# Optimization experiments

Measured on AMD Instinct MI355X. Metric: run time of the kernel, lower is better.

The kernel has to match this reference:

```python
import jax, jax.numpy as jnp
import numpy as np

N_SRC, N_DST, E = 100000, 50000, 1000000
IN_F, H, D = 256, 4, 32
NEG_SLOPE = 0.2


def setup_inputs() -> dict:
    key = jax.random.key(0)
    k = jax.random.split(key, 7)
    x = jax.random.normal(k[0], (N_SRC, IN_F), dtype=jnp.float32)
    # scale weights so exp() of attention logits stays well-conditioned
    fc_w = jax.random.normal(k[1], (H * D, IN_F), dtype=jnp.float32) * (1.0 / np.sqrt(IN_F))
    attn_l = jax.random.normal(k[2], (1, H, D), dtype=jnp.float32) * 0.1
    attn_r = jax.random.normal(k[3], (1, H, D), dtype=jnp.float32) * 0.1
    src_idx = jax.random.randint(k[4], (E,), 0, N_SRC, dtype=jnp.int32)
    dst_idx = jax.random.randint(k[5], (E,), 0, N_DST, dtype=jnp.int32)
    dst_node_ids = jax.random.randint(k[6], (N_DST,), 0, N_SRC, dtype=jnp.int32)
    return {"x": x, "fc_w": fc_w, "attn_l": attn_l, "attn_r": attn_r,
            "src_idx": src_idx, "dst_idx": dst_idx, "dst_node_ids": dst_node_ids}


def reference(x, fc_w, attn_l, attn_r, src_idx, dst_idx, dst_node_ids):
    # fc: [N_src, in] @ [in, H*D] -> [N_src, H, D]
    h = (x @ fc_w.T).reshape(-1, H, D)
    # per-node, per-head attention scalars
    el = jnp.einsum('nhd,ohd->nh', h, attn_l)            # [N_src, H]
    h_dst = h[dst_node_ids]                               # self_gather -> [N_dst, H, D]
    er = jnp.einsum('nhd,ohd->nh', h_dst, attn_r)        # [N_dst, H]
    # apply_edge: e = el[src] + er[dst], then leaky_relu + exp (edge softmax numerator)
    e = el[src_idx] + er[dst_idx]                         # [E, H]
    e = jnp.where(e >= 0, e, NEG_SLOPE * e)
    exp_e = jnp.exp(e)
    # apply_node: segment-sum denominators over destination nodes
    sum_exp = jax.ops.segment_sum(exp_e, dst_idx, num_segments=N_DST)  # [N_dst, H]
    att = exp_e / sum_exp[dst_idx]                        # [E, H]
    # attention_gather: weighted scatter-add of source features to dst nodes
    msg = att[:, :, None] * h[src_idx]                    # [E, H, D]
    out = jax.ops.segment_sum(msg, dst_idx, num_segments=N_DST)        # [N_dst, H, D]
    return out.reshape(N_DST, H * D)
```

## Files before the change

### kernel.cpp

```cpp
#include <hip/hip_runtime.h>
#include <hip/hip_bf16.h>

#define N_SRC_N  100000
#define N_DST_N  50000
#define NE       1000000
#define IN_F     256
#define NH       4
#define ND       32
#define HD       128
#define NEG_SLOPE 0.2f

#define DPB      32
#define NB       1563
#define CAP      1024

typedef __attribute__((ext_vector_type(8))) short short8v;
typedef __attribute__((ext_vector_type(4))) short short4v;
typedef __attribute__((ext_vector_type(4))) float f32x4;

__device__ __forceinline__ short f2bf(float f) {
    __hip_bfloat16 h = __float2bfloat16(f);
    return *reinterpret_cast<short*>(&h);
}
__device__ __forceinline__ float bflo(unsigned u) { return __uint_as_float(u << 16); }
__device__ __forceinline__ float bfhi(unsigned u) { return __uint_as_float(u & 0xffff0000u); }

__device__ __forceinline__ void gl_lds16(const float* g, float* l) {
    __builtin_amdgcn_global_load_lds((const __attribute__((address_space(1))) unsigned*)g,
                                     (__attribute__((address_space(3))) unsigned*)l,
                                     16, 0, 0);
}

__global__ __launch_bounds__(256) void cvt_w(const float* __restrict__ w,
                                             short* __restrict__ wb)
{
    int i4 = blockIdx.x * 256 + threadIdx.x;
    if (i4 < (HD * IN_F) / 4) {
        f32x4 v = ((const f32x4*)w)[i4];
        short4v s;
        s[0] = f2bf(v[0]); s[1] = f2bf(v[1]); s[2] = f2bf(v[2]); s[3] = f2bf(v[3]);
        ((short4v*)wb)[i4] = s;
    }
}

__global__ __launch_bounds__(256) void gemm_fc_mfma(
    const float* __restrict__ x, const short* __restrict__ wb,
    const float* __restrict__ al, short* __restrict__ hb,
    float* __restrict__ el, int nrows)
{
    __shared__ float lds[2][64 * 64];

    const int w  = threadIdx.x >> 6;
    const int l  = threadIdx.x & 63;
    const int lr = l & 15;
    const int lk = l >> 4;
    const int row0 = blockIdx.x * 64;

    short8v bfr[2][8];
#pragma unroll
    for (int ct = 0; ct < 2; ++ct)
#pragma unroll
        for (int k = 0; k < 8; ++k)
            bfr[ct][k] = *(const short8v*)(wb + (size_t)(w * 32 + ct * 16 + lr) * IN_F
                                              + lk * 8 + k * 32);

    f32x4 acc[4][2];
#pragma unroll
    for (int rt = 0; rt < 4; ++rt)
#pragma unroll
        for (int ct = 0; ct < 2; ++ct) acc[rt][ct] = (f32x4){0.f, 0.f, 0.f, 0.f};

    auto stage = [&](int buf, int k0) {
#pragma unroll
        for (int i = 0; i < 4; ++i) {
            int chunk = i * 4 + w;
            int row   = chunk * 4 + (l >> 4);
            int srow  = row0 + row; if (srow > nrows - 1) srow = nrows - 1;
            int c_pos = (l & 15) * 16;
            int c_src = c_pos ^ ((row & 7) << 5);
            const float* g = x + (size_t)srow * IN_F + k0 + (c_src >> 2);
            gl_lds16(g, &lds[buf][chunk * 256]);
        }
    };

    stage(0, 0);
#pragma unroll
    for (int t = 0; t < 4; ++t) {
        __syncthreads();
        if (t < 3) stage((t + 1) & 1, (t + 1) * 64);
        const float* Lb = lds[t & 1];
#pragma unroll
        for (int kc = 0; kc < 2; ++kc) {
#pragma unroll
            for (int rt = 0; rt < 4; ++rt) {
                int row = rt * 16 + lr;
                int cb  = (kc * 128 + lk * 32) ^ ((row & 7) << 5);
                const float* p = Lb + row * 64 + (cb >> 2);
                f32x4 u0 = *(const f32x4*)p;
                f32x4 u1 = *(const f32x4*)(p + 4);
                short8v af;
                af[0] = f2bf(u0[0]); af[1] = f2bf(u0[1]);
                af[2] = f2bf(u0[2]); af[3] = f2bf(u0[3]);
                af[4] = f2bf(u1[0]); af[5] = f2bf(u1[1]);
                af[6] = f2bf(u1[2]); af[7] = f2bf(u1[3]);
                acc[rt][0] = __builtin_amdgcn_mfma_f32_16x16x32_bf16(
                                 af, bfr[0][t * 2 + kc], acc[rt][0], 0, 0, 0);
                acc[rt][1] = __builtin_amdgcn_mfma_f32_16x16x32_bf16(
                                 af, bfr[1][t * 2 + kc], acc[rt][1], 0, 0, 0);
            }
        }
    }

#pragma unroll
    for (int rt = 0; rt < 4; ++rt)
#pragma unroll
        for (int r = 0; r < 4; ++r) {
            int row = row0 + rt * 16 + lk * 4 + r;
            if (row < nrows) {
                short* hp = hb + (size_t)row * HD + w * 32 + lr;
                hp[0]  = f2bf(acc[rt][0][r]);
                hp[16] = f2bf(acc[rt][1][r]);
            }
        }

    float al0 = al[w * 32 + lr], al1 = al[w * 32 + 16 + lr];
#pragma unroll
    for (int rt = 0; rt < 4; ++rt) {
        float p[4];
#pragma unroll
        for (int r = 0; r < 4; ++r)
            p[r] = acc[rt][0][r] * al0 + acc[rt][1][r] * al1;
#pragma unroll
        for (int o = 1; o < 16; o <<= 1) {
#pragma unroll
            for (int r = 0; r < 4; ++r) p[r] += __shfl_xor(p[r], o, 64);
        }
        if (lr == 0) {
#pragma unroll
            for (int r = 0; r < 4; ++r) {
                int row = row0 + rt * 16 + lk * 4 + r;
                if (row < nrows) el[row * NH + w] = p[r];
            }
        }
    }
}

__global__ __launch_bounds__(256) void er_kernel(
    const short* __restrict__ hb, const float* __restrict__ ar,
    const int* __restrict__ dnid, float* __restrict__ er, int ndst)
{
    int i = blockIdx.x * 4 + (threadIdx.x >> 6);
    if (i >= ndst) return;
    int l = threadIdx.x & 63;
    int n = dnid[i];
    unsigned u = *(const unsigned*)(hb + (size_t)n * HD + 2 * l);
    float s = bflo(u) * ar[2 * l] + bfhi(u) * ar[2 * l + 1];
#pragma unroll
    for (int o = 1; o < 16; o <<= 1) s += __shfl_xor(s, o, 64);
    if ((l & 15) == 0) er[i * NH + (l >> 4)] = s;
}

__global__ __launch_bounds__(256) void bucket_hist(
    const int4* __restrict__ dst4, int* __restrict__ bcnt, int n4)
{
    __shared__ int lh[NB];
    for (int i = threadIdx.x; i < NB; i += 256) lh[i] = 0;
    __syncthreads();
#pragma unroll
    for (int q = 0; q < 4; ++q) {
        int e4 = blockIdx.x * 1024 + q * 256 + threadIdx.x;
        if (e4 < n4) {
            int4 v = dst4[e4];
            atomicAdd(&lh[v.x >> 5], 1); atomicAdd(&lh[v.y >> 5], 1);
            atomicAdd(&lh[v.z >> 5], 1); atomicAdd(&lh[v.w >> 5], 1);
        }
    }
    __syncthreads();
    for (int i = threadIdx.x; i < NB; i += 256) {
        int c = lh[i];
        if (c > 0) atomicAdd(&bcnt[i], c);
    }
}

__global__ __launch_bounds__(1024) void bucket_scan(
    const int* __restrict__ bcnt, int* __restrict__ boff, int* __restrict__ bcur, int n)
{
    int tid = threadIdx.x;
    int i0 = 2 * tid, i1 = 2 * tid + 1;
    int a = (i0 < n) ? bcnt[i0] : 0;
    int c = (i1 < n) ? bcnt[i1] : 0;
    int s = a + c, v = s;
#pragma unroll
    for (int o = 1; o < 64; o <<= 1) {
        int t = __shfl_up(v, o, 64);
        if ((tid & 63) >= o) v += t;
    }
    __shared__ int ws[16];
    if ((tid & 63) == 63) ws[tid >> 6] = v;
    __syncthreads();
    int add = 0;
    for (int q = 0; q < (tid >> 6); ++q) add += ws[q];
    int excl = v - s + add;
    if (i0 < n) { boff[i0] = excl;     bcur[i0] = excl; }
    if (i1 < n) { boff[i1] = excl + a; bcur[i1] = excl + a; }
}

__global__ __launch_bounds__(256) void partition(
    const int4* __restrict__ src4, const int4* __restrict__ dst4,
    int* __restrict__ bcur, int* __restrict__ ebuf, int n4)
{
    __shared__ int lh[NB];
    __shared__ int base[NB];
    for (int i = threadIdx.x; i < NB; i += 256) lh[i] = 0;
    __syncthreads();
    int4 sv[4], dv[4];
#pragma unroll
    for (int q = 0; q < 4; ++q) {
        int e4 = blockIdx.x * 1024 + q * 256 + threadIdx.x;
        if (e4 < n4) {
            sv[q] = src4[e4]; dv[q] = dst4[e4];
            atomicAdd(&lh[dv[q].x >> 5], 1); atomicAdd(&lh[dv[q].y >> 5], 1);
            atomicAdd(&lh[dv[q].z >> 5], 1); atomicAdd(&lh[dv[q].w >> 5], 1);
        } else {
            dv[q].x = -1;
        }
    }
    __syncthreads();
    for (int i = threadIdx.x; i < NB; i += 256) {
        int cnt = lh[i];
        base[i] = (cnt > 0) ? atomicAdd(&bcur[i], cnt) : 0;
        lh[i] = 0;
    }
    __syncthreads();
#pragma unroll
    for (int q = 0; q < 4; ++q) {
        if (dv[q].x < 0) continue;
        int ss[4] = {sv[q].x, sv[q].y, sv[q].z, sv[q].w};
        int dd[4] = {dv[q].x, dv[q].y, dv[q].z, dv[q].w};
#pragma unroll
        for (int j = 0; j < 4; ++j) {
            int b = dd[j] >> 5;
            int off = atomicAdd(&lh[b], 1);
            ebuf[base[b] + off] = ss[j] | ((dd[j] & 31) << 17);
        }
    }
}

__global__ __launch_bounds__(256) void gat_gather(
    const short* __restrict__ hb, const float* __restrict__ el,
    const float* __restrict__ er, const int* __restrict__ ebuf,
    const int* __restrict__ bcnt, const int* __restrict__ boff,
    float* __restrict__ out, int ndst)
{
    __shared__ int stage_[CAP];
    __shared__ int ssrc[CAP];
    __shared__ int lh[DPB];
    __shared__ int loff[DPB + 1];
    __shared__ int curs[DPB];

    const int b = blockIdx.x;
    const int tid = threadIdx.x;
    const int cnt = bcnt[b];
    const int gbase = boff[b];
    const int lcnt = (cnt < CAP) ? cnt : CAP;

    if (tid < DPB) lh[tid] = 0;
    __syncthreads();
    for (int i = tid; i < lcnt; i += 256) {
        int p = ebuf[gbase + i];
        stage_[i] = p;
        atomicAdd(&lh[(p >> 17) & 31], 1);
    }
    __syncthreads();
    if (tid < DPB) {
        int v = lh[tid];
#pragma unroll
        for (int o = 1; o < 32; o <<= 1) {
            int t = __shfl_up(v, o, 64);
            if (tid >= o) v += t;
        }
        loff[tid + 1] = v;
        if (tid == 0) loff[0] = 0;
    }
    __syncthreads();
    if (tid < DPB) curs[tid] = loff[tid];
    __syncthreads();
    for (int i = tid; i < lcnt; i += 256) {
        int p = stage_[i];
        int dl = (p >> 17) & 31;
        int pos = atomicAdd(&curs[dl], 1);
        ssrc[pos] = p & 0x1FFFF;
    }
    __syncthreads();

    const int wv = tid >> 6;
    const int l  = tid & 63;
    const int head = l >> 4;

    for (int dl = wv; dl < DPB; dl += 4) {
        int d = b * DPB + dl;
        if (d >= ndst) continue;
        int j0 = loff[dl], j1 = loff[dl + 1];
        float erv = er[d * NH + head];

        float sumA = 0.f, sumB = 0.f;
        float acc0A = 0.f, acc1A = 0.f, acc0B = 0.f, acc1B = 0.f;
        int j = j0;
        for (; j + 2 <= j1; j += 2) {
            int s0 = ssrc[j], s1 = ssrc[j + 1];
            unsigned u0 = *(const unsigned*)(hb + (size_t)s0 * HD + 2 * l);
            unsigned u1 = *(const unsigned*)(hb + (size_t)s1 * HD + 2 * l);
            float e0 = el[s0 * NH + head] + erv;
            float e1 = el[s1 * NH + head] + erv;
            e0 = (e0 >= 0.f) ? e0 : NEG_SLOPE * e0;
            e1 = (e1 >= 0.f) ? e1 : NEG_SLOPE * e1;
            float w0 = __expf(e0), w1 = __expf(e1);
            sumA += w0; sumB += w1;
            acc0A = fmaf(w0, bflo(u0), acc0A); acc1A = fmaf(w0, bfhi(u0), acc1A);
            acc0B = fmaf(w1, bflo(u1), acc0B); acc1B = fmaf(w1, bfhi(u1), acc1B);
        }
        if (j < j1) {
            int s0 = ssrc[j];
            unsigned u0 = *(const unsigned*)(hb + (size_t)s0 * HD + 2 * l);
            float e0 = el[s0 * NH + head] + erv;
            e0 = (e0 >= 0.f) ? e0 : NEG_SLOPE * e0;
            float w0 = __expf(e0);
            sumA += w0;
            acc0A = fmaf(w0, bflo(u0), acc0A); acc1A = fmaf(w0, bfhi(u0), acc1A);
        }
        if (cnt > CAP) {
            for (int t = CAP; t < cnt; ++t) {
                int p = ebuf[gbase + t];
                if (((p >> 17) & 31) == dl) {
                    int s0 = p & 0x1FFFF;
                    unsigned u0 = *(const unsigned*)(hb + (size_t)s0 * HD + 2 * l);
                    float e0 = el[s0 * NH + head] + erv;
                    e0 = (e0 >= 0.f) ? e0 : NEG_SLOPE * e0;
                    float w0 = __expf(e0);
                    sumA += w0;
                    acc0A = fmaf(w0, bflo(u0), acc0A); acc1A = fmaf(w0, bfhi(u0), acc1A);
                }
            }
        }
        float sum = sumA + sumB;
        bool any = (j1 > j0) || (cnt > CAP);
        float inv = any ? 1.f / sum : 0.f;
        float2 o2 = make_float2((acc0A + acc0B) * inv, (acc1A + acc1B) * inv);
        *(float2*)(out + (size_t)d * HD + 2 * l) = o2;
    }
}

extern "C" void kernel_launch(void* const* d_in, const int* in_sizes, int n_in,
                              void* d_out, int out_size, void* d_ws, size_t ws_size,
                              hipStream_t stream)
{
    const float* x   = (const float*)d_in[0];
    const float* fw  = (const float*)d_in[1];
    const float* al  = (const float*)d_in[2];
    const float* ar  = (const float*)d_in[3];
    const int*   src = (const int*)d_in[4];
    const int*   dst = (const int*)d_in[5];
    const int*   dnid= (const int*)d_in[6];
    float* out = (float*)d_out;

    char* ws = (char*)d_ws;
    size_t off = 0;
    auto alloc = [&](size_t bytes) -> void* {
        void* p = ws + off;
        off = (off + bytes + 255) & ~(size_t)255;
        return p;
    };
    short* hb   = (short*)alloc((size_t)N_SRC_N * HD * sizeof(short));
    short* wb   = (short*)alloc((size_t)HD * IN_F * sizeof(short));
    float* el   = (float*)alloc((size_t)N_SRC_N * NH * sizeof(float));
    float* er   = (float*)alloc((size_t)N_DST_N * NH * sizeof(float));
    int*   ebuf = (int*)alloc((size_t)NE * sizeof(int));
    int*   bcnt = (int*)alloc((size_t)NB * sizeof(int));
    int*   boff = (int*)alloc((size_t)NB * sizeof(int));
    int*   bcur = (int*)alloc((size_t)NB * sizeof(int));

    hipMemsetAsync(bcnt, 0, (size_t)NB * sizeof(int), stream);

    cvt_w<<<(HD * IN_F / 4 + 255) / 256, 256, 0, stream>>>(fw, wb);
    gemm_fc_mfma<<<(N_SRC_N + 63) / 64, 256, 0, stream>>>(x, wb, al, hb, el, N_SRC_N);
    er_kernel<<<(N_DST_N + 3) / 4, 256, 0, stream>>>(hb, ar, dnid, er, N_DST_N);
    bucket_hist<<<(NE / 4 + 1023) / 1024, 256, 0, stream>>>((const int4*)dst, bcnt, NE / 4);
    bucket_scan<<<1, 1024, 0, stream>>>(bcnt, boff, bcur, NB);
    partition<<<(NE / 4 + 1023) / 1024, 256, 0, stream>>>((const int4*)src, (const int4*)dst,
                                                          bcur, ebuf, NE / 4);
    gat_gather<<<NB, 256, 0, stream>>>(hb, el, er, ebuf, bcnt, boff, out, N_DST_N);
}
```

Baseline: 137.4 us.

## Prefetch all GEMM K-tiles upfront, widen gather blocks, unroll edge loop by 8

The FC GEMM now issues async loads for all four K-tiles into four LDS buffers at once, then waits on each in turn with graded vmcnt waits instead of double-buffering. This exposes more memory-level parallelism at the cost of 64KB of LDS per block, which may reduce occupancy. The gather kernel moves to 512 threads, eight waves covering the 32 destinations per block. Its edge loop is unrolled by 8 so more independent feature gathers are in flight, which raises register pressure.

```diff
diff --git a/kernel.cpp b/kernel.cpp
--- a/kernel.cpp
+++ b/kernel.cpp
@@ -48,7 +48,7 @@
     const float* __restrict__ al, short* __restrict__ hb,
     float* __restrict__ el, int nrows)
 {
-    __shared__ float lds[2][64 * 64];
+    __shared__ float lds[4][64 * 64];
 
     const int w  = threadIdx.x >> 6;
     const int l  = threadIdx.x & 63;
@@ -64,13 +64,8 @@
             bfr[ct][k] = *(const short8v*)(wb + (size_t)(w * 32 + ct * 16 + lr) * IN_F
                                               + lk * 8 + k * 32);
 
-    f32x4 acc[4][2];
-#pragma unroll
-    for (int rt = 0; rt < 4; ++rt)
-#pragma unroll
-        for (int ct = 0; ct < 2; ++ct) acc[rt][ct] = (f32x4){0.f, 0.f, 0.f, 0.f};
-
-    auto stage = [&](int buf, int k0) {
+#pragma unroll
+    for (int t = 0; t < 4; ++t) {
 #pragma unroll
         for (int i = 0; i < 4; ++i) {
             int chunk = i * 4 + w;
@@ -78,38 +73,47 @@
             int srow  = row0 + row; if (srow > nrows - 1) srow = nrows - 1;
             int c_pos = (l & 15) * 16;
             int c_src = c_pos ^ ((row & 7) << 5);
-            const float* g = x + (size_t)srow * IN_F + k0 + (c_src >> 2);
-            gl_lds16(g, &lds[buf][chunk * 256]);
-        }
-    };
-
-    stage(0, 0);
-#pragma unroll
-    for (int t = 0; t < 4; ++t) {
-        __syncthreads();
-        if (t < 3) stage((t + 1) & 1, (t + 1) * 64);
-        const float* Lb = lds[t & 1];
-#pragma unroll
-        for (int kc = 0; kc < 2; ++kc) {
-#pragma unroll
-            for (int rt = 0; rt < 4; ++rt) {
-                int row = rt * 16 + lr;
-                int cb  = (kc * 128 + lk * 32) ^ ((row & 7) << 5);
-                const float* p = Lb + row * 64 + (cb >> 2);
-                f32x4 u0 = *(const f32x4*)p;
-                f32x4 u1 = *(const f32x4*)(p + 4);
-                short8v af;
-                af[0] = f2bf(u0[0]); af[1] = f2bf(u0[1]);
-                af[2] = f2bf(u0[2]); af[3] = f2bf(u0[3]);
-                af[4] = f2bf(u1[0]); af[5] = f2bf(u1[1]);
-                af[6] = f2bf(u1[2]); af[7] = f2bf(u1[3]);
-                acc[rt][0] = __builtin_amdgcn_mfma_f32_16x16x32_bf16(
-                                 af, bfr[0][t * 2 + kc], acc[rt][0], 0, 0, 0);
-                acc[rt][1] = __builtin_amdgcn_mfma_f32_16x16x32_bf16(
-                                 af, bfr[1][t * 2 + kc], acc[rt][1], 0, 0, 0);
-            }
-        }
-    }
+            const float* g = x + (size_t)srow * IN_F + t * 64 + (c_src >> 2);
+            gl_lds16(g, &lds[t][chunk * 256]);
+        }
+    }
+
+    f32x4 acc[4][2];
+#pragma unroll
+    for (int rt = 0; rt < 4; ++rt)
+#pragma unroll
+        for (int ct = 0; ct < 2; ++ct) acc[rt][ct] = (f32x4){0.f, 0.f, 0.f, 0.f};
+
+#define GEMM_TILE(T, N)                                                           \
+    asm volatile("s_waitcnt vmcnt(" #N ")" ::: "memory");                         \
+    __builtin_amdgcn_s_barrier();                                                 \
+    __builtin_amdgcn_sched_barrier(0);                                            \
+    _Pragma("unroll")                                                             \
+    for (int kc = 0; kc < 2; ++kc) {                                              \
+        _Pragma("unroll")                                                         \
+        for (int rt = 0; rt < 4; ++rt) {                                          \
+            int row = rt * 16 + lr;                                               \
+            int cb  = (kc * 128 + lk * 32) ^ ((row & 7) << 5);                    \
+            const float* p = &lds[T][0] + row * 64 + (cb >> 2);                   \
+            f32x4 u0 = *(const f32x4*)p;                                          \
+            f32x4 u1 = *(const f32x4*)(p + 4);                                    \
+            short8v af;                                                           \
+            af[0] = f2bf(u0[0]); af[1] = f2bf(u0[1]);                             \
+            af[2] = f2bf(u0[2]); af[3] = f2bf(u0[3]);                             \
+            af[4] = f2bf(u1[0]); af[5] = f2bf(u1[1]);                             \
+            af[6] = f2bf(u1[2]); af[7] = f2bf(u1[3]);                             \
+            acc[rt][0] = __builtin_amdgcn_mfma_f32_16x16x32_bf16(                 \
+                             af, bfr[0][(T) * 2 + kc], acc[rt][0], 0, 0, 0);      \
+            acc[rt][1] = __builtin_amdgcn_mfma_f32_16x16x32_bf16(                 \
+                             af, bfr[1][(T) * 2 + kc], acc[rt][1], 0, 0, 0);      \
+        }                                                                         \
+    }
+
+    GEMM_TILE(0, 12)
+    GEMM_TILE(1, 8)
+    GEMM_TILE(2, 4)
+    GEMM_TILE(3, 0)
+#undef GEMM_TILE
 
 #pragma unroll
     for (int rt = 0; rt < 4; ++rt)
@@ -246,7 +250,7 @@
     }
 }
 
-__global__ __launch_bounds__(256) void gat_gather(
+__global__ __launch_bounds__(512) void gat_gather(
     const short* __restrict__ hb, const float* __restrict__ el,
     const float* __restrict__ er, const int* __restrict__ ebuf,
     const int* __restrict__ bcnt, const int* __restrict__ boff,
@@ -266,7 +270,7 @@
 
     if (tid < DPB) lh[tid] = 0;
     __syncthreads();
-    for (int i = tid; i < lcnt; i += 256) {
+    for (int i = tid; i < lcnt; i += 512) {
         int p = ebuf[gbase + i];
         stage_[i] = p;
         atomicAdd(&lh[(p >> 17) & 31], 1);
@@ -285,7 +289,7 @@
     __syncthreads();
     if (tid < DPB) curs[tid] = loff[tid];
     __syncthreads();
-    for (int i = tid; i < lcnt; i += 256) {
+    for (int i = tid; i < lcnt; i += 512) {
         int p = stage_[i];
         int dl = (p >> 17) & 31;
         int pos = atomicAdd(&curs[dl], 1);
@@ -297,7 +301,7 @@
     const int l  = tid & 63;
     const int head = l >> 4;
 
-    for (int dl = wv; dl < DPB; dl += 4) {
+    for (int dl = wv; dl < DPB; dl += 8) {
         int d = b * DPB + dl;
         if (d >= ndst) continue;
         int j0 = loff[dl], j1 = loff[dl + 1];
@@ -306,6 +310,31 @@
         float sumA = 0.f, sumB = 0.f;
         float acc0A = 0.f, acc1A = 0.f, acc0B = 0.f, acc1B = 0.f;
         int j = j0;
+        for (; j + 8 <= j1; j += 8) {
+            int s[8]; unsigned u[8]; float e[8];
+#pragma unroll
+            for (int q = 0; q < 8; ++q) s[q] = ssrc[j + q];
+#pragma unroll
+            for (int q = 0; q < 8; ++q)
+                u[q] = *(const unsigned*)(hb + (size_t)s[q] * HD + 2 * l);
+#pragma unroll
+            for (int q = 0; q < 8; ++q) e[q] = el[s[q] * NH + head];
+#pragma unroll
+            for (int q = 0; q < 8; ++q) {
+                float ev = e[q] + erv;
+                ev = (ev >= 0.f) ? ev : NEG_SLOPE * ev;
+                float wq = __expf(ev);
+                if (q & 1) {
+                    sumB += wq;
+                    acc0B = fmaf(wq, bflo(u[q]), acc0B);
+                    acc1B = fmaf(wq, bfhi(u[q]), acc1B);
+                } else {
+                    sumA += wq;
+                    acc0A = fmaf(wq, bflo(u[q]), acc0A);
+                    acc1A = fmaf(wq, bfhi(u[q]), acc1A);
+                }
+            }
+        }
         for (; j + 2 <= j1; j += 2) {
             int s0 = ssrc[j], s1 = ssrc[j + 1];
             unsigned u0 = *(const unsigned*)(hb + (size_t)s0 * HD + 2 * l);
@@ -388,5 +417,5 @@
     bucket_scan<<<1, 1024, 0, stream>>>(bcnt, boff, bcur, NB);
     partition<<<(NE / 4 + 1023) / 1024, 256, 0, stream>>>((const int4*)src, (const int4*)dst,
                                                           bcur, ebuf, NE / 4);
-    gat_gather<<<NB, 256, 0, stream>>>(hb, el, er, ebuf, bcnt, boff, out, N_DST_N);
-}
+    gat_gather<<<NB, 512, 0, stream>>>(hb, el, er, ebuf, bcnt, boff, out, N_DST_N);
+}
```

Result: no change. 139.9 us (+1.8%).

## Restructure FC GEMM into persistent 160-row blocks with 4-deep LDS ring pipeline

Applied to the files above, without the earlier changes.

The FC GEMM kernel now processes 160 rows per block as ten 16-row steps through a 4-slot LDS ring. Global loads for a step are issued three steps ahead and waited on with explicit vmcnt counts, instead of the previous two-buffer scheme over K for 64 rows. Each step computes the full K=256 for 16 rows and writes out h and el. This aims to hide global load latency and amortise the weight-fragment loads over more rows. Bounds checks were removed, so correctness depends on N_SRC being exactly 625*160. The hand-tuned waitcnt values are fragile if the compiler emits other memory ops.

```diff
diff --git a/kernel.cpp b/kernel.cpp
--- a/kernel.cpp
+++ b/kernel.cpp
@@ -30,6 +30,7 @@
                                      (__attribute__((address_space(3))) unsigned*)l,
                                      16, 0, 0);
 }
+#define SB0() __builtin_amdgcn_sched_barrier(0)
 
 __global__ __launch_bounds__(256) void cvt_w(const float* __restrict__ w,
                                              short* __restrict__ wb)
@@ -46,103 +47,102 @@
 __global__ __launch_bounds__(256) void gemm_fc_mfma(
     const float* __restrict__ x, const short* __restrict__ wb,
     const float* __restrict__ al, short* __restrict__ hb,
-    float* __restrict__ el, int nrows)
-{
-    __shared__ float lds[2][64 * 64];
+    float* __restrict__ el)
+{
+    __shared__ float ring[4][16 * 256];
 
     const int w  = threadIdx.x >> 6;
     const int l  = threadIdx.x & 63;
     const int lr = l & 15;
     const int lk = l >> 4;
-    const int row0 = blockIdx.x * 64;
+    const int row00 = blockIdx.x * 160;
 
     short8v bfr[2][8];
 #pragma unroll
     for (int ct = 0; ct < 2; ++ct)
 #pragma unroll
-        for (int k = 0; k < 8; ++k)
-            bfr[ct][k] = *(const short8v*)(wb + (size_t)(w * 32 + ct * 16 + lr) * IN_F
-                                              + lk * 8 + k * 32);
-
-    f32x4 acc[4][2];
-#pragma unroll
-    for (int rt = 0; rt < 4; ++rt)
-#pragma unroll
-        for (int ct = 0; ct < 2; ++ct) acc[rt][ct] = (f32x4){0.f, 0.f, 0.f, 0.f};
-
-    auto stage = [&](int buf, int k0) {
-#pragma unroll
-        for (int i = 0; i < 4; ++i) {
-            int chunk = i * 4 + w;
-            int row   = chunk * 4 + (l >> 4);
-            int srow  = row0 + row; if (srow > nrows - 1) srow = nrows - 1;
-            int c_pos = (l & 15) * 16;
-            int c_src = c_pos ^ ((row & 7) << 5);
-            const float* g = x + (size_t)srow * IN_F + k0 + (c_src >> 2);
-            gl_lds16(g, &lds[buf][chunk * 256]);
-        }
-    };
-
-    stage(0, 0);
-#pragma unroll
-    for (int t = 0; t < 4; ++t) {
-        __syncthreads();
-        if (t < 3) stage((t + 1) & 1, (t + 1) * 64);
-        const float* Lb = lds[t & 1];
-#pragma unroll
-        for (int kc = 0; kc < 2; ++kc) {
-#pragma unroll
-            for (int rt = 0; rt < 4; ++rt) {
-                int row = rt * 16 + lr;
-                int cb  = (kc * 128 + lk * 32) ^ ((row & 7) << 5);
-                const float* p = Lb + row * 64 + (cb >> 2);
-                f32x4 u0 = *(const f32x4*)p;
-                f32x4 u1 = *(const f32x4*)(p + 4);
-                short8v af;
-                af[0] = f2bf(u0[0]); af[1] = f2bf(u0[1]);
-                af[2] = f2bf(u0[2]); af[3] = f2bf(u0[3]);
-                af[4] = f2bf(u1[0]); af[5] = f2bf(u1[1]);
-                af[6] = f2bf(u1[2]); af[7] = f2bf(u1[3]);
-                acc[rt][0] = __builtin_amdgcn_mfma_f32_16x16x32_bf16(
-                                 af, bfr[0][t * 2 + kc], acc[rt][0], 0, 0, 0);
-                acc[rt][1] = __builtin_amdgcn_mfma_f32_16x16x32_bf16(
-                                 af, bfr[1][t * 2 + kc], acc[rt][1], 0, 0, 0);
-            }
-        }
-    }
-
-#pragma unroll
-    for (int rt = 0; rt < 4; ++rt)
-#pragma unroll
-        for (int r = 0; r < 4; ++r) {
-            int row = row0 + rt * 16 + lk * 4 + r;
-            if (row < nrows) {
-                short* hp = hb + (size_t)row * HD + w * 32 + lr;
-                hp[0]  = f2bf(acc[rt][0][r]);
-                hp[16] = f2bf(acc[rt][1][r]);
-            }
-        }
-
-    float al0 = al[w * 32 + lr], al1 = al[w * 32 + 16 + lr];
-#pragma unroll
-    for (int rt = 0; rt < 4; ++rt) {
-        float p[4];
-#pragma unroll
-        for (int r = 0; r < 4; ++r)
-            p[r] = acc[rt][0][r] * al0 + acc[rt][1][r] * al1;
-#pragma unroll
-        for (int o = 1; o < 16; o <<= 1) {
-#pragma unroll
-            for (int r = 0; r < 4; ++r) p[r] += __shfl_xor(p[r], o, 64);
-        }
-        if (lr == 0) {
-#pragma unroll
-            for (int r = 0; r < 4; ++r) {
-                int row = row0 + rt * 16 + lk * 4 + r;
-                if (row < nrows) el[row * NH + w] = p[r];
-            }
-        }
-    }
+        for (int kk = 0; kk < 8; ++kk)
+            bfr[ct][kk] = *(const short8v*)(wb + (size_t)(w * 32 + ct * 16 + lr) * IN_F
+                                               + kk * 32 + lk * 8);
+    SB0();
+
+#define STAGE(T)                                                              \
+    {                                                                         \
+        _Pragma("unroll")                                                     \
+        for (int i = 0; i < 4; ++i) {                                         \
+            int chunk = w * 4 + i;                                            \
+            int srow  = row00 + (T) * 16 + chunk;                             \
+            int csrc  = (l * 16) ^ ((chunk & 7) << 4);                        \
+            gl_lds16(x + (size_t)srow * IN_F + (csrc >> 2),                   \
+                     &ring[(T) & 3][chunk * 256]);                            \
+        }                                                                     \
+        SB0();                                                                \
+    }
+
+    STAGE(0) STAGE(1) STAGE(2)
+
+    const float al0 = al[w * 32 + lr], al1 = al[w * 32 + 16 + lr];
+
+#define GSTEP(T, NXT, NW)                                                     \
+    {                                                                         \
+        if ((NXT) >= 0) STAGE((NXT) < 0 ? 0 : (NXT))                          \
+        asm volatile("s_waitcnt vmcnt(" #NW ")" ::: "memory");                \
+        __builtin_amdgcn_s_barrier();                                         \
+        SB0();                                                                \
+        f32x4 a0 = {0.f, 0.f, 0.f, 0.f}, a1 = {0.f, 0.f, 0.f, 0.f};          \
+        const char* rb = (const char*)&ring[(T) & 3][lr * 256];               \
+        _Pragma("unroll")                                                     \
+        for (int kk = 0; kk < 8; ++kk) {                                      \
+            int b0 = (kk * 128 + lk * 32) ^ ((lr & 7) << 4);                  \
+            f32x4 u0 = *(const f32x4*)(rb + b0);                              \
+            f32x4 u1 = *(const f32x4*)(rb + (b0 ^ 16));                       \
+            short8v af;                                                       \
+            af[0] = f2bf(u0[0]); af[1] = f2bf(u0[1]);                         \
+            af[2] = f2bf(u0[2]); af[3] = f2bf(u0[3]);                         \
+            af[4] = f2bf(u1[0]); af[5] = f2bf(u1[1]);                         \
+            af[6] = f2bf(u1[2]); af[7] = f2bf(u1[3]);                         \
+            a0 = __builtin_amdgcn_mfma_f32_16x16x32_bf16(af, bfr[0][kk], a0, 0, 0, 0); \
+            a1 = __builtin_amdgcn_mfma_f32_16x16x32_bf16(af, bfr[1][kk], a1, 0, 0, 0); \
+        }                                                                     \
+        _Pragma("unroll")                                                     \
+        for (int r = 0; r < 4; ++r) {                                         \
+            int row = row00 + (T) * 16 + lk * 4 + r;                          \
+            short* hp = hb + (size_t)row * HD + w * 32 + lr;                  \
+            hp[0]  = f2bf(a0[r]);                                             \
+            hp[16] = f2bf(a1[r]);                                             \
+        }                                                                     \
+        float p0 = a0[0] * al0 + a1[0] * al1;                                 \
+        float p1 = a0[1] * al0 + a1[1] * al1;                                 \
+        float p2 = a0[2] * al0 + a1[2] * al1;                                 \
+        float p3 = a0[3] * al0 + a1[3] * al1;                                 \
+        _Pragma("unroll")                                                     \
+        for (int o = 1; o < 16; o <<= 1) {                                    \
+            p0 += __shfl_xor(p0, o, 64); p1 += __shfl_xor(p1, o, 64);         \
+            p2 += __shfl_xor(p2, o, 64); p3 += __shfl_xor(p3, o, 64);         \
+        }                                                                     \
+        if (lr == 0) {                                                        \
+            int rowe = row00 + (T) * 16 + lk * 4;                             \
+            el[(rowe + 0) * NH + w] = p0;                                     \
+            el[(rowe + 1) * NH + w] = p1;                                     \
+            el[(rowe + 2) * NH + w] = p2;                                     \
+            el[(rowe + 3) * NH + w] = p3;                                     \
+        }                                                                     \
+        SB0();                                                                \
+        __builtin_amdgcn_s_barrier();                                         \
+    }
+
+    GSTEP(0, 3, 12)
+    GSTEP(1, 4, 20)
+    GSTEP(2, 5, 28)
+    GSTEP(3, 6, 36)
+    GSTEP(4, 7, 36)
+    GSTEP(5, 8, 36)
+    GSTEP(6, 9, 36)
+    GSTEP(7, -1, 28)
+    GSTEP(8, -1, 28)
+    GSTEP(9, -1, 24)
+#undef GSTEP
+#undef STAGE
 }
 
 __global__ __launch_bounds__(256) void er_kernel(
@@ -382,7 +382,7 @@
     hipMemsetAsync(bcnt, 0, (size_t)NB * sizeof(int), stream);
 
     cvt_w<<<(HD * IN_F / 4 + 255) / 256, 256, 0, stream>>>(fw, wb);
-    gemm_fc_mfma<<<(N_SRC_N + 63) / 64, 256, 0, stream>>>(x, wb, al, hb, el, N_SRC_N);
+    gemm_fc_mfma<<<625, 256, 0, stream>>>(x, wb, al, hb, el);
     er_kernel<<<(N_DST_N + 3) / 4, 256, 0, stream>>>(hb, ar, dnid, er, N_DST_N);
     bucket_hist<<<(NE / 4 + 1023) / 1024, 256, 0, stream>>>((const int4*)dst, bcnt, NE / 4);
     bucket_scan<<<1, 1024, 0, stream>>>(bcnt, boff, bcur, NB);
```

After: 135.3 us. Within noise of the previous version (-1.6%).

## Make FC GEMM persistent with LDS-resident weights and fold log2e into logits

Applied to the files above, without the earlier changes.

The FC GEMM becomes a persistent kernel of 512 blocks. Each block loads the full bf16 weight matrix into swizzled LDS once. Each wave then loops over 16-row tiles, loading x directly from global into registers and computing all 128 output columns. This replaces the old layout of 64-row tiles with per-wave weight fragments in registers and double-buffered global-to-LDS staging of x. Separately, the el and er logits are prescaled by log2(e), so the edge loop uses exp2f and a fmax-based leaky ReLU, dropping a multiply per edge. The risks are 64KB of LDS per block limiting occupancy and reduced latency hiding for the direct x loads.

```diff
diff --git a/kernel.cpp b/kernel.cpp
--- a/kernel.cpp
+++ b/kernel.cpp
@@ -9,6 +9,7 @@
 #define ND       32
 #define HD       128
 #define NEG_SLOPE 0.2f
+#define L2E      1.44269504f
 
 #define DPB      32
 #define NB       1563
@@ -24,12 +25,6 @@
 }
 __device__ __forceinline__ float bflo(unsigned u) { return __uint_as_float(u << 16); }
 __device__ __forceinline__ float bfhi(unsigned u) { return __uint_as_float(u & 0xffff0000u); }
-
-__device__ __forceinline__ void gl_lds16(const float* g, float* l) {
-    __builtin_amdgcn_global_load_lds((const __attribute__((address_space(1))) unsigned*)g,
-                                     (__attribute__((address_space(3))) unsigned*)l,
-                                     16, 0, 0);
-}
 
 __global__ __launch_bounds__(256) void cvt_w(const float* __restrict__ w,
                                              short* __restrict__ wb)
@@ -46,100 +41,88 @@
 __global__ __launch_bounds__(256) void gemm_fc_mfma(
     const float* __restrict__ x, const short* __restrict__ wb,
     const float* __restrict__ al, short* __restrict__ hb,
-    float* __restrict__ el, int nrows)
-{
-    __shared__ float lds[2][64 * 64];
-
-    const int w  = threadIdx.x >> 6;
-    const int l  = threadIdx.x & 63;
+    float* __restrict__ el)
+{
+    __shared__ short wlds[HD * IN_F];
+
+    const int tid = threadIdx.x;
+    {
+        int row = tid >> 1, half = tid & 1;
+#pragma unroll
+        for (int c = 0; c < 16; ++c) {
+            int chunk = half * 16 + c;
+            short8v v = *(const short8v*)(wb + row * IN_F + chunk * 8);
+            int boff = (chunk * 16) ^ ((row & 7) << 4);
+            *(short8v*)((char*)wlds + row * 512 + boff) = v;
+        }
+    }
+    __syncthreads();
+
+    const int w  = tid >> 6;
+    const int l  = tid & 63;
     const int lr = l & 15;
     const int lk = l >> 4;
-    const int row0 = blockIdx.x * 64;
-
-    short8v bfr[2][8];
-#pragma unroll
-    for (int ct = 0; ct < 2; ++ct)
-#pragma unroll
-        for (int k = 0; k < 8; ++k)
-            bfr[ct][k] = *(const short8v*)(wb + (size_t)(w * 32 + ct * 16 + lr) * IN_F
-                                              + lk * 8 + k * 32);
-
-    f32x4 acc[4][2];
-#pragma unroll
-    for (int rt = 0; rt < 4; ++rt)
-#pragma unroll
-        for (int ct = 0; ct < 2; ++ct) acc[rt][ct] = (f32x4){0.f, 0.f, 0.f, 0.f};
-
-    auto stage = [&](int buf, int k0) {
-#pragma unroll
-        for (int i = 0; i < 4; ++i) {
-            int chunk = i * 4 + w;
-            int row   = chunk * 4 + (l >> 4);
-            int srow  = row0 + row; if (srow > nrows - 1) srow = nrows - 1;
-            int c_pos = (l & 15) * 16;
-            int c_src = c_pos ^ ((row & 7) << 5);
-            const float* g = x + (size_t)srow * IN_F + k0 + (c_src >> 2);
-            gl_lds16(g, &lds[buf][chunk * 256]);
-        }
-    };
-
-    stage(0, 0);
-#pragma unroll
-    for (int t = 0; t < 4; ++t) {
-        __syncthreads();
-        if (t < 3) stage((t + 1) & 1, (t + 1) * 64);
-        const float* Lb = lds[t & 1];
-#pragma unroll
-        for (int kc = 0; kc < 2; ++kc) {
-#pragma unroll
-            for (int rt = 0; rt < 4; ++rt) {
-                int row = rt * 16 + lr;
-                int cb  = (kc * 128 + lk * 32) ^ ((row & 7) << 5);
-                const float* p = Lb + row * 64 + (cb >> 2);
-                f32x4 u0 = *(const f32x4*)p;
-                f32x4 u1 = *(const f32x4*)(p + 4);
-                short8v af;
-                af[0] = f2bf(u0[0]); af[1] = f2bf(u0[1]);
-                af[2] = f2bf(u0[2]); af[3] = f2bf(u0[3]);
-                af[4] = f2bf(u1[0]); af[5] = f2bf(u1[1]);
-                af[6] = f2bf(u1[2]); af[7] = f2bf(u1[3]);
-                acc[rt][0] = __builtin_amdgcn_mfma_f32_16x16x32_bf16(
-                                 af, bfr[0][t * 2 + kc], acc[rt][0], 0, 0, 0);
-                acc[rt][1] = __builtin_amdgcn_mfma_f32_16x16x32_bf16(
-                                 af, bfr[1][t * 2 + kc], acc[rt][1], 0, 0, 0);
+
+    float alv[8];
+#pragma unroll
+    for (int ct = 0; ct < 8; ++ct) alv[ct] = al[ct * 16 + lr] * L2E;
+
+    const int wave_id = blockIdx.x * 4 + w;
+    for (int tile = wave_id; tile < N_SRC_N / 16; tile += 2048) {
+        const int row0 = tile * 16;
+        const float* xp = x + (size_t)(row0 + lr) * IN_F + lk * 8;
+
+        f32x4 a[16];
+#pragma unroll
+        for (int kk = 0; kk < 8; ++kk) {
+            a[2 * kk]     = *(const f32x4*)(xp + kk * 32);
+            a[2 * kk + 1] = *(const f32x4*)(xp + kk * 32 + 4);
+        }
+        __builtin_amdgcn_sched_barrier(0);
+
+        f32x4 acc[8];
+#pragma unroll
+        for (int ct = 0; ct < 8; ++ct) acc[ct] = (f32x4){0.f, 0.f, 0.f, 0.f};
+
+#pragma unroll
+        for (int kk = 0; kk < 8; ++kk) {
+            f32x4 u0 = a[2 * kk], u1 = a[2 * kk + 1];
+            short8v af;
+            af[0] = f2bf(u0[0]); af[1] = f2bf(u0[1]);
+            af[2] = f2bf(u0[2]); af[3] = f2bf(u0[3]);
+            af[4] = f2bf(u1[0]); af[5] = f2bf(u1[1]);
+            af[6] = f2bf(u1[2]); af[7] = f2bf(u1[3]);
+            const int boff = (kk * 64 + lk * 16) ^ ((lr & 7) << 4);
+#pragma unroll
+            for (int ct = 0; ct < 8; ++ct) {
+                short8v bf = *(const short8v*)((const char*)wlds
+                                               + (ct * 16 + lr) * 512 + boff);
+                acc[ct] = __builtin_amdgcn_mfma_f32_16x16x32_bf16(af, bf, acc[ct], 0, 0, 0);
             }
         }
-    }
-
-#pragma unroll
-    for (int rt = 0; rt < 4; ++rt)
+
 #pragma unroll
         for (int r = 0; r < 4; ++r) {
-            int row = row0 + rt * 16 + lk * 4 + r;
-            if (row < nrows) {
-                short* hp = hb + (size_t)row * HD + w * 32 + lr;
-                hp[0]  = f2bf(acc[rt][0][r]);
-                hp[16] = f2bf(acc[rt][1][r]);
+            short* hp = hb + (size_t)(row0 + lk * 4 + r) * HD + lr;
+#pragma unroll
+            for (int ct = 0; ct < 8; ++ct) hp[ct * 16] = f2bf(acc[ct][r]);
+        }
+
+#pragma unroll
+        for (int h = 0; h < 4; ++h) {
+            float p[4];
+#pragma unroll
+            for (int r = 0; r < 4; ++r)
+                p[r] = acc[2 * h][r] * alv[2 * h] + acc[2 * h + 1][r] * alv[2 * h + 1];
+#pragma unroll
+            for (int o = 1; o < 16; o <<= 1) {
+#pragma unroll
+                for (int r = 0; r < 4; ++r) p[r] += __shfl_xor(p[r], o, 64);
             }
-        }
-
-    float al0 = al[w * 32 + lr], al1 = al[w * 32 + 16 + lr];
-#pragma unroll
-    for (int rt = 0; rt < 4; ++rt) {
-        float p[4];
-#pragma unroll
-        for (int r = 0; r < 4; ++r)
-            p[r] = acc[rt][0][r] * al0 + acc[rt][1][r] * al1;
-#pragma unroll
-        for (int o = 1; o < 16; o <<= 1) {
-#pragma unroll
-            for (int r = 0; r < 4; ++r) p[r] += __shfl_xor(p[r], o, 64);
-        }
-        if (lr == 0) {
-#pragma unroll
-            for (int r = 0; r < 4; ++r) {
-                int row = row0 + rt * 16 + lk * 4 + r;
-                if (row < nrows) el[row * NH + w] = p[r];
+            if (lr == 0) {
+#pragma unroll
+                for (int r = 0; r < 4; ++r)
+                    el[(row0 + lk * 4 + r) * NH + h] = p[r];
             }
         }
     }
@@ -157,7 +140,7 @@
     float s = bflo(u) * ar[2 * l] + bfhi(u) * ar[2 * l + 1];
 #pragma unroll
     for (int o = 1; o < 16; o <<= 1) s += __shfl_xor(s, o, 64);
-    if ((l & 15) == 0) er[i * NH + (l >> 4)] = s;
+    if ((l & 15) == 0) er[i * NH + (l >> 4)] = s * L2E;
 }
 
 __global__ __launch_bounds__(256) void bucket_hist(
@@ -312,9 +295,9 @@
             unsigned u1 = *(const unsigned*)(hb + (size_t)s1 * HD + 2 * l);
             float e0 = el[s0 * NH + head] + erv;
             float e1 = el[s1 * NH + head] + erv;
-            e0 = (e0 >= 0.f) ? e0 : NEG_SLOPE * e0;
-            e1 = (e1 >= 0.f) ? e1 : NEG_SLOPE * e1;
-            float w0 = __expf(e0), w1 = __expf(e1);
+            e0 = fmaxf(e0, NEG_SLOPE * e0);
+            e1 = fmaxf(e1, NEG_SLOPE * e1);
+            float w0 = exp2f(e0), w1 = exp2f(e1);
             sumA += w0; sumB += w1;
             acc0A = fmaf(w0, bflo(u0), acc0A); acc1A = fmaf(w0, bfhi(u0), acc1A);
             acc0B = fmaf(w1, bflo(u1), acc0B); acc1B = fmaf(w1, bfhi(u1), acc1B);
@@ -323,8 +306,8 @@
             int s0 = ssrc[j];
             unsigned u0 = *(const unsigned*)(hb + (size_t)s0 * HD + 2 * l);
             float e0 = el[s0 * NH + head] + erv;
-            e0 = (e0 >= 0.f) ? e0 : NEG_SLOPE * e0;
-            float w0 = __expf(e0);
+            e0 = fmaxf(e0, NEG_SLOPE * e0);
+            float w0 = exp2f(e0);
             sumA += w0;
             acc0A = fmaf(w0, bflo(u0), acc0A); acc1A = fmaf(w0, bfhi(u0), acc1A);
         }
@@ -335,8 +318,8 @@
                     int s0 = p & 0x1FFFF;
                     unsigned u0 = *(const unsigned*)(hb + (size_t)s0 * HD + 2 * l);
                     float e0 = el[s0 * NH + head] + erv;
-                    e0 = (e0 >= 0.f) ? e0 : NEG_SLOPE * e0;
-                    float w0 = __expf(e0);
+                    e0 = fmaxf(e0, NEG_SLOPE * e0);
+                    float w0 = exp2f(e0);
                     sumA += w0;
                     acc0A = fmaf(w0, bflo(u0), acc0A); acc1A = fmaf(w0, bfhi(u0), acc1A);
                 }
@@ -382,7 +365,7 @@
     hipMemsetAsync(bcnt, 0, (size_t)NB * sizeof(int), stream);
 
     cvt_w<<<(HD * IN_F / 4 + 255) / 256, 256, 0, stream>>>(fw, wb);
-    gemm_fc_mfma<<<(N_SRC_N + 63) / 64, 256, 0, stream>>>(x, wb, al, hb, el, N_SRC_N);
+    gemm_fc_mfma<<<512, 256, 0, stream>>>(x, wb, al, hb, el);
     er_kernel<<<(N_DST_N + 3) / 4, 256, 0, stream>>>(hb, ar, dnid, er, N_DST_N);
     bucket_hist<<<(NE / 4 + 1023) / 1024, 256, 0, stream>>>((const int4*)dst, bcnt, NE / 4);
     bucket_scan<<<1, 1024, 0, stream>>>(bcnt, boff, bcur, NB);
```

After: 142.2 us. +3.5%, slower.
